# Kernel tuning notes

Measured on AMD Instinct MI355X. Metric: run time of the kernel, lower is better.

Reference implementation:

```python
import jax, jax.numpy as jnp
import numpy as np

B, N, D = 8, 2048, 256
SCALE = 10.0  # self.scale_constant

def setup_inputs() -> dict:
    key = jax.random.key(0)
    ks = jax.random.split(key, 8)
    x = jax.random.normal(ks[0], (B, N, D), dtype=jnp.float32)
    recycler_mask = jax.random.randint(ks[1], (N, N), 0, 2, dtype=jnp.int32)
    s = 1.0 / np.sqrt(D)
    Wq = jax.random.uniform(ks[2], (D, D), jnp.float32, -s, s)
    bq = jax.random.uniform(ks[3], (D,), jnp.float32, -s, s)
    Wk = jax.random.uniform(ks[4], (D, D), jnp.float32, -s, s)
    bk = jax.random.uniform(ks[5], (D,), jnp.float32, -s, s)
    Wl = jax.random.uniform(ks[6], (1, D), jnp.float32, -s, s)
    bl = jax.random.uniform(ks[7], (1,), jnp.float32, -s, s)
    return {"x": x, "recycler_mask": recycler_mask, "Wq": Wq, "bq": bq,
            "Wk": Wk, "bk": bk, "Wl": Wl, "bl": bl}

def reference(x, recycler_mask, Wq, bq, Wk, bk, Wl, bl):
    # query/key linear projections (torch Linear: x @ W.T + b)
    query = jnp.einsum('bnd,ed->bne', x, Wq) + bq  # (B,N,D)
    key_ = jnp.einsum('bnd,ed->bne', x, Wk) + bk   # (B,N,D)
    scores = jnp.einsum('bnd,bmd->bnm', query, key_)  # (B,N,N)
    scores = SCALE * jnp.tanh(scores)
    scores = jnp.where(recycler_mask[None, :, :] == 0, -jnp.inf, scores)
    picked_logit = jnp.einsum('bnd,ed->bne', x, Wl) + bl  # (B,N,1)
    return picked_logit, scores
```

## Files before the change

### kernel.cpp

```cpp
#include <hip/hip_runtime.h>
#include <math.h>

#define B_ 8
#define N_ 2048
#define D_ 256
#define SCALE_ 10.0f
#define NEG_SENTINEL_ (-1.0e30f)

#define BM 128
#define BN 128
#define BK 64
#define KTILES (D_ / BK)
#define TILE_ELEMS (BM * BK)

typedef unsigned short ushort_t;
typedef __attribute__((ext_vector_type(8))) short bf16x8;
typedef __attribute__((ext_vector_type(4))) float f32x4;

__device__ __forceinline__ ushort_t f2bf(float f) {
    union { float f; unsigned int u; } a; a.f = f;
    unsigned int r = a.u + 0x7fffu + ((a.u >> 16) & 1u);
    return (ushort_t)(r >> 16);
}

__device__ __forceinline__ void gl16(const void* g, void* l) {
    __builtin_amdgcn_global_load_lds(
        (const __attribute__((address_space(1))) unsigned int*)g,
        (__attribute__((address_space(3))) unsigned int*)l, 16, 0, 0);
}

__global__ __launch_bounds__(256) void rcy_proj_v4(
    const float* __restrict__ x,
    const float* __restrict__ Wq, const float* __restrict__ bq,
    const float* __restrict__ Wk, const float* __restrict__ bk,
    ushort_t* __restrict__ Qo, ushort_t* __restrict__ Ko)
{
    __shared__ ushort_t As[BM * BK];
    __shared__ ushort_t Bs[BN * BK];

    const float* W  = blockIdx.z ? Wk : Wq;
    const float* bi = blockIdx.z ? bk : bq;
    ushort_t* out   = blockIdx.z ? Ko : Qo;

    const int m0 = blockIdx.x * BM;
    const int n0 = blockIdx.y * BN;
    const int t  = threadIdx.x;
    const int w  = t >> 6, l = t & 63;
    const int wr = w >> 1, wc = w & 1;
    const int srow0 = t >> 3;
    const int schunk = t & 7;

    f32x4 acc[4][4] = {};

    for (int k0 = 0; k0 < D_; k0 += BK) {
        __syncthreads();
        #pragma unroll
        for (int p = 0; p < 4; ++p) {
            const int row = p * 32 + srow0;
            const float4* xa = (const float4*)(x + (size_t)(m0 + row) * D_ + k0 + schunk * 8);
            float4 f0 = xa[0], f1 = xa[1];
            union { bf16x8 v; ushort_t u[8]; } pa;
            pa.u[0]=f2bf(f0.x); pa.u[1]=f2bf(f0.y); pa.u[2]=f2bf(f0.z); pa.u[3]=f2bf(f0.w);
            pa.u[4]=f2bf(f1.x); pa.u[5]=f2bf(f1.y); pa.u[6]=f2bf(f1.z); pa.u[7]=f2bf(f1.w);
            const float4* wa = (const float4*)(W + (size_t)(n0 + row) * D_ + k0 + schunk * 8);
            float4 g0 = wa[0], g1 = wa[1];
            union { bf16x8 v; ushort_t u[8]; } pb;
            pb.u[0]=f2bf(g0.x); pb.u[1]=f2bf(g0.y); pb.u[2]=f2bf(g0.z); pb.u[3]=f2bf(g0.w);
            pb.u[4]=f2bf(g1.x); pb.u[5]=f2bf(g1.y); pb.u[6]=f2bf(g1.z); pb.u[7]=f2bf(g1.w);
            const int off = ((row * 128 + schunk * 16) ^ ((row & 7) << 4));
            *(bf16x8*)((char*)As + off) = pa.v;
            *(bf16x8*)((char*)Bs + off) = pb.v;
        }
        __syncthreads();
        #pragma unroll
        for (int ks = 0; ks < 2; ++ks) {
            bf16x8 af[4], bf[4];
            #pragma unroll
            for (int f = 0; f < 4; ++f) {
                const int m = wr * 64 + f * 16 + (l & 15);
                af[f] = *(const bf16x8*)((const char*)As +
                          ((m * 128 + ks * 64 + (l >> 4) * 16) ^ ((m & 7) << 4)));
                const int n = wc * 64 + f * 16 + (l & 15);
                bf[f] = *(const bf16x8*)((const char*)Bs +
                          ((n * 128 + ks * 64 + (l >> 4) * 16) ^ ((n & 7) << 4)));
            }
            #pragma unroll
            for (int i = 0; i < 4; ++i)
                #pragma unroll
                for (int j = 0; j < 4; ++j)
                    acc[i][j] = __builtin_amdgcn_mfma_f32_16x16x32_bf16(af[i], bf[j], acc[i][j], 0, 0, 0);
        }
    }

    const int b  = m0 >> 11;
    const int rb = (m0 & 2047) >> 7;
    const size_t tbase = (((size_t)b * 16 + rb) * KTILES + (blockIdx.y * 2 + wc)) * (size_t)TILE_ELEMS;
    #pragma unroll
    for (int j = 0; j < 4; ++j) {
        const int col = n0 + wc * 64 + j * 16 + (l & 15);
        const float bv = bi[col];
        const int cl = j * 16 + (l & 15);
        #pragma unroll
        for (int i = 0; i < 4; ++i) {
            #pragma unroll
            for (int r = 0; r < 4; ++r) {
                const int rl = wr * 64 + i * 16 + (l >> 4) * 4 + r;
                out[tbase + (size_t)rl * BK + cl] = f2bf(acc[i][j][r] + bv);
            }
        }
    }
}

__global__ __launch_bounds__(256) void rcy_scores_v4(
    const ushort_t* __restrict__ Qt, const ushort_t* __restrict__ Kt,
    const int* __restrict__ mask, float* __restrict__ out)
{
    __shared__ ushort_t lds[2][2][TILE_ELEMS];

    const int bz = blockIdx.z;
    const int bx = blockIdx.x;
    const int by = blockIdx.y;
    const int t  = threadIdx.x;
    const int w  = t >> 6, l = t & 63;
    const int wr = w >> 1, wc = w & 1;

    const char* gA = (const char*)(Qt + (((size_t)bz * 16 + bx) * KTILES) * TILE_ELEMS);
    const char* gB = (const char*)(Kt + (((size_t)bz * 16 + by) * KTILES) * TILE_ELEMS);

    f32x4 acc[4][4] = {};

    #define STAGE(buf, kb) { \
        const char* sa = gA + (size_t)(kb) * (TILE_ELEMS * 2); \
        const char* sb = gB + (size_t)(kb) * (TILE_ELEMS * 2); \
        char* la = (char*)&lds[buf][0][0]; \
        char* lb = (char*)&lds[buf][1][0]; \
        _Pragma("unroll") \
        for (int q = 0; q < 4; ++q) { \
            gl16(sa + q * 4096 + t * 16, la + q * 4096 + t * 16); \
            gl16(sb + q * 4096 + t * 16, lb + q * 4096 + t * 16); \
        } }

    #define COMPUTE(buf) { \
        const ushort_t* As_ = &lds[buf][0][0]; \
        const ushort_t* Bs_ = &lds[buf][1][0]; \
        _Pragma("unroll") \
        for (int ks = 0; ks < 2; ++ks) { \
            bf16x8 af[4], bf[4]; \
            _Pragma("unroll") \
            for (int f = 0; f < 4; ++f) { \
                const int m = wr * 64 + f * 16 + (l & 15); \
                af[f] = *(const bf16x8*)(As_ + m * BK + ks * 32 + (l >> 4) * 8); \
                const int n = wc * 64 + f * 16 + (l & 15); \
                bf[f] = *(const bf16x8*)(Bs_ + n * BK + ks * 32 + (l >> 4) * 8); \
            } \
            _Pragma("unroll") \
            for (int i = 0; i < 4; ++i) \
                _Pragma("unroll") \
                for (int j = 0; j < 4; ++j) \
                    acc[i][j] = __builtin_amdgcn_mfma_f32_16x16x32_bf16(af[i], bf[j], acc[i][j], 0, 0, 0); \
        } }

    STAGE(0, 0);
    __syncthreads();
    STAGE(1, 1);
    COMPUTE(0);
    __syncthreads();
    STAGE(0, 2);
    COMPUTE(1);
    __syncthreads();
    STAGE(1, 3);
    COMPUTE(0);
    __syncthreads();
    COMPUTE(1);

    const int bm0 = bx * BM, bn0 = by * BN;
    float* outb = out + (size_t)bz * N_ * N_;
    #pragma unroll
    for (int i = 0; i < 4; ++i) {
        #pragma unroll
        for (int r = 0; r < 4; ++r) {
            const int row = bm0 + wr * 64 + i * 16 + (l >> 4) * 4 + r;
            #pragma unroll
            for (int j = 0; j < 4; ++j) {
                const int col = bn0 + wc * 64 + j * 16 + (l & 15);
                const int mk = mask[(size_t)row * N_ + col];
                const float v = acc[i][j][r];
                const float e = __expf(v + v);
                const float s = fmaf(-20.0f, __builtin_amdgcn_rcpf(e + 1.0f), SCALE_);
                outb[(size_t)row * N_ + col] = mk ? s : NEG_SENTINEL_;
            }
        }
    }
    #undef STAGE
    #undef COMPUTE
}

__global__ __launch_bounds__(256) void rcy_logit_v2(
    const float* __restrict__ x, const float* __restrict__ Wl,
    const float* __restrict__ bl, float* __restrict__ out)
{
    const int lane = threadIdx.x & 63;
    const int wv   = threadIdx.x >> 6;
    const int row  = (blockIdx.x << 2) + wv;
    const float* xr = x + (size_t)row * D_;
    float4 v = *(const float4*)&xr[lane << 2];
    float4 wt = *(const float4*)&Wl[lane << 2];
    float s = v.x*wt.x + v.y*wt.y + v.z*wt.z + v.w*wt.w;
    #pragma unroll
    for (int off = 32; off > 0; off >>= 1) s += __shfl_down(s, off);
    if (lane == 0) out[row] = s + bl[0];
}

extern "C" void kernel_launch(void* const* d_in, const int* in_sizes, int n_in,
                              void* d_out, int out_size, void* d_ws, size_t ws_size,
                              hipStream_t stream)
{
    const float* x  = (const float*)d_in[0];
    const int* mask = (const int*)d_in[1];
    const float* Wq = (const float*)d_in[2];
    const float* bq = (const float*)d_in[3];
    const float* Wk = (const float*)d_in[4];
    const float* bk = (const float*)d_in[5];
    const float* Wl = (const float*)d_in[6];
    const float* bl = (const float*)d_in[7];

    float* logit  = (float*)d_out;
    float* scores = (float*)d_out + (size_t)B_ * N_;

    ushort_t* Qw = (ushort_t*)d_ws;
    ushort_t* Kw = Qw + (size_t)B_ * 16 * KTILES * TILE_ELEMS;

    rcy_proj_v4<<<dim3((B_*N_)/BM, D_/BN, 2), 256, 0, stream>>>(x, Wq, bq, Wk, bk, Qw, Kw);
    rcy_scores_v4<<<dim3(N_/BM, N_/BN, B_), 256, 0, stream>>>(Qw, Kw, mask, scores);
    rcy_logit_v2<<<dim3((B_*N_)/4), 256, 0, stream>>>(x, Wl, bl, logit);
}
```

Baseline: 67.68 us.

## Fuse Q/K projections and logit into one kernel, reorder scores grid, nontemporal I/O

```diff
diff --git a/kernel.cpp b/kernel.cpp
--- a/kernel.cpp
+++ b/kernel.cpp
@@ -29,18 +29,17 @@
         (__attribute__((address_space(3))) unsigned int*)l, 16, 0, 0);
 }
 
-__global__ __launch_bounds__(256) void rcy_proj_v4(
+__global__ __launch_bounds__(256) void rcy_proj_v5(
     const float* __restrict__ x,
     const float* __restrict__ Wq, const float* __restrict__ bq,
     const float* __restrict__ Wk, const float* __restrict__ bk,
-    ushort_t* __restrict__ Qo, ushort_t* __restrict__ Ko)
+    const float* __restrict__ Wl, const float* __restrict__ bl,
+    ushort_t* __restrict__ Qo, ushort_t* __restrict__ Ko,
+    float* __restrict__ logit)
 {
     __shared__ ushort_t As[BM * BK];
-    __shared__ ushort_t Bs[BN * BK];
-
-    const float* W  = blockIdx.z ? Wk : Wq;
-    const float* bi = blockIdx.z ? bk : bq;
-    ushort_t* out   = blockIdx.z ? Ko : Qo;
+    __shared__ ushort_t Bqs[BN * BK];
+    __shared__ ushort_t Bks[BN * BK];
 
     const int m0 = blockIdx.x * BM;
     const int n0 = blockIdx.y * BN;
@@ -49,46 +48,67 @@
     const int wr = w >> 1, wc = w & 1;
     const int srow0 = t >> 3;
     const int schunk = t & 7;
-
-    f32x4 acc[4][4] = {};
+    const bool do_logit = (blockIdx.y == 0);
+
+    f32x4 accq[4][4] = {};
+    f32x4 acck[4][4] = {};
+    float lacc[4] = {0.f, 0.f, 0.f, 0.f};
 
     for (int k0 = 0; k0 < D_; k0 += BK) {
         __syncthreads();
+        float4 wl0, wl1;
+        if (do_logit) {
+            const float4* wlp = (const float4*)(Wl + k0 + schunk * 8);
+            wl0 = wlp[0]; wl1 = wlp[1];
+        }
         #pragma unroll
         for (int p = 0; p < 4; ++p) {
             const int row = p * 32 + srow0;
+            const int off = ((row * 128 + schunk * 16) ^ ((row & 7) << 4));
             const float4* xa = (const float4*)(x + (size_t)(m0 + row) * D_ + k0 + schunk * 8);
             float4 f0 = xa[0], f1 = xa[1];
             union { bf16x8 v; ushort_t u[8]; } pa;
             pa.u[0]=f2bf(f0.x); pa.u[1]=f2bf(f0.y); pa.u[2]=f2bf(f0.z); pa.u[3]=f2bf(f0.w);
             pa.u[4]=f2bf(f1.x); pa.u[5]=f2bf(f1.y); pa.u[6]=f2bf(f1.z); pa.u[7]=f2bf(f1.w);
-            const float4* wa = (const float4*)(W + (size_t)(n0 + row) * D_ + k0 + schunk * 8);
-            float4 g0 = wa[0], g1 = wa[1];
+            *(bf16x8*)((char*)As + off) = pa.v;
+            if (do_logit) {
+                lacc[p] += f0.x*wl0.x + f0.y*wl0.y + f0.z*wl0.z + f0.w*wl0.w
+                         + f1.x*wl1.x + f1.y*wl1.y + f1.z*wl1.z + f1.w*wl1.w;
+            }
+            const float4* qa = (const float4*)(Wq + (size_t)(n0 + row) * D_ + k0 + schunk * 8);
+            float4 g0 = qa[0], g1 = qa[1];
             union { bf16x8 v; ushort_t u[8]; } pb;
             pb.u[0]=f2bf(g0.x); pb.u[1]=f2bf(g0.y); pb.u[2]=f2bf(g0.z); pb.u[3]=f2bf(g0.w);
             pb.u[4]=f2bf(g1.x); pb.u[5]=f2bf(g1.y); pb.u[6]=f2bf(g1.z); pb.u[7]=f2bf(g1.w);
-            const int off = ((row * 128 + schunk * 16) ^ ((row & 7) << 4));
-            *(bf16x8*)((char*)As + off) = pa.v;
-            *(bf16x8*)((char*)Bs + off) = pb.v;
+            *(bf16x8*)((char*)Bqs + off) = pb.v;
+            const float4* ka = (const float4*)(Wk + (size_t)(n0 + row) * D_ + k0 + schunk * 8);
+            float4 h0 = ka[0], h1 = ka[1];
+            union { bf16x8 v; ushort_t u[8]; } pc;
+            pc.u[0]=f2bf(h0.x); pc.u[1]=f2bf(h0.y); pc.u[2]=f2bf(h0.z); pc.u[3]=f2bf(h0.w);
+            pc.u[4]=f2bf(h1.x); pc.u[5]=f2bf(h1.y); pc.u[6]=f2bf(h1.z); pc.u[7]=f2bf(h1.w);
+            *(bf16x8*)((char*)Bks + off) = pc.v;
         }
         __syncthreads();
         #pragma unroll
         for (int ks = 0; ks < 2; ++ks) {
-            bf16x8 af[4], bf[4];
+            bf16x8 af[4], bqf[4], bkf[4];
             #pragma unroll
             for (int f = 0; f < 4; ++f) {
                 const int m = wr * 64 + f * 16 + (l & 15);
-                af[f] = *(const bf16x8*)((const char*)As +
-                          ((m * 128 + ks * 64 + (l >> 4) * 16) ^ ((m & 7) << 4)));
+                const int aoff = ((m * 128 + ks * 64 + (l >> 4) * 16) ^ ((m & 7) << 4));
+                af[f] = *(const bf16x8*)((const char*)As + aoff);
                 const int n = wc * 64 + f * 16 + (l & 15);
-                bf[f] = *(const bf16x8*)((const char*)Bs +
-                          ((n * 128 + ks * 64 + (l >> 4) * 16) ^ ((n & 7) << 4)));
+                const int boff = ((n * 128 + ks * 64 + (l >> 4) * 16) ^ ((n & 7) << 4));
+                bqf[f] = *(const bf16x8*)((const char*)Bqs + boff);
+                bkf[f] = *(const bf16x8*)((const char*)Bks + boff);
             }
             #pragma unroll
             for (int i = 0; i < 4; ++i)
                 #pragma unroll
-                for (int j = 0; j < 4; ++j)
-                    acc[i][j] = __builtin_amdgcn_mfma_f32_16x16x32_bf16(af[i], bf[j], acc[i][j], 0, 0, 0);
+                for (int j = 0; j < 4; ++j) {
+                    accq[i][j] = __builtin_amdgcn_mfma_f32_16x16x32_bf16(af[i], bqf[j], accq[i][j], 0, 0, 0);
+                    acck[i][j] = __builtin_amdgcn_mfma_f32_16x16x32_bf16(af[i], bkf[j], acck[i][j], 0, 0, 0);
+                }
         }
     }
 
@@ -98,28 +118,44 @@
     #pragma unroll
     for (int j = 0; j < 4; ++j) {
         const int col = n0 + wc * 64 + j * 16 + (l & 15);
-        const float bv = bi[col];
+        const float bvq = bq[col];
+        const float bvk = bk[col];
         const int cl = j * 16 + (l & 15);
         #pragma unroll
         for (int i = 0; i < 4; ++i) {
             #pragma unroll
             for (int r = 0; r < 4; ++r) {
                 const int rl = wr * 64 + i * 16 + (l >> 4) * 4 + r;
-                out[tbase + (size_t)rl * BK + cl] = f2bf(acc[i][j][r] + bv);
-            }
-        }
-    }
-}
-
-__global__ __launch_bounds__(256) void rcy_scores_v4(
+                Qo[tbase + (size_t)rl * BK + cl] = f2bf(accq[i][j][r] + bvq);
+                Ko[tbase + (size_t)rl * BK + cl] = f2bf(acck[i][j][r] + bvk);
+            }
+        }
+    }
+
+    if (do_logit) {
+        const float bl0 = bl[0];
+        #pragma unroll
+        for (int p = 0; p < 4; ++p) {
+            float s = lacc[p];
+            s += __shfl_down(s, 4);
+            s += __shfl_down(s, 2);
+            s += __shfl_down(s, 1);
+            if (schunk == 0) logit[m0 + p * 32 + srow0] = s + bl0;
+        }
+    }
+}
+
+__global__ __launch_bounds__(256) void rcy_scores_v5(
     const ushort_t* __restrict__ Qt, const ushort_t* __restrict__ Kt,
     const int* __restrict__ mask, float* __restrict__ out)
 {
     __shared__ ushort_t lds[2][2][TILE_ELEMS];
 
-    const int bz = blockIdx.z;
-    const int bx = blockIdx.x;
-    const int by = blockIdx.y;
+    const int g  = blockIdx.x;
+    const int bz = g & 7;
+    const int r_ = g >> 3;
+    const int by = r_ >> 4;
+    const int bx = r_ & 15;
     const int t  = threadIdx.x;
     const int w  = t >> 6, l = t & 63;
     const int wr = w >> 1, wc = w & 1;
@@ -183,32 +219,17 @@
             #pragma unroll
             for (int j = 0; j < 4; ++j) {
                 const int col = bn0 + wc * 64 + j * 16 + (l & 15);
-                const int mk = mask[(size_t)row * N_ + col];
+                const int mk = __builtin_nontemporal_load(&mask[(size_t)row * N_ + col]);
                 const float v = acc[i][j][r];
                 const float e = __expf(v + v);
                 const float s = fmaf(-20.0f, __builtin_amdgcn_rcpf(e + 1.0f), SCALE_);
-                outb[(size_t)row * N_ + col] = mk ? s : NEG_SENTINEL_;
+                __builtin_nontemporal_store(mk ? s : NEG_SENTINEL_,
+                                            &outb[(size_t)row * N_ + col]);
             }
         }
     }
     #undef STAGE
     #undef COMPUTE
-}
-
-__global__ __launch_bounds__(256) void rcy_logit_v2(
-    const float* __restrict__ x, const float* __restrict__ Wl,
-    const float* __restrict__ bl, float* __restrict__ out)
-{
-    const int lane = threadIdx.x & 63;
-    const int wv   = threadIdx.x >> 6;
-    const int row  = (blockIdx.x << 2) + wv;
-    const float* xr = x + (size_t)row * D_;
-    float4 v = *(const float4*)&xr[lane << 2];
-    float4 wt = *(const float4*)&Wl[lane << 2];
-    float s = v.x*wt.x + v.y*wt.y + v.z*wt.z + v.w*wt.w;
-    #pragma unroll
-    for (int off = 32; off > 0; off >>= 1) s += __shfl_down(s, off);
-    if (lane == 0) out[row] = s + bl[0];
 }
 
 extern "C" void kernel_launch(void* const* d_in, const int* in_sizes, int n_in,
@@ -230,7 +251,7 @@
     ushort_t* Qw = (ushort_t*)d_ws;
     ushort_t* Kw = Qw + (size_t)B_ * 16 * KTILES * TILE_ELEMS;
 
-    rcy_proj_v4<<<dim3((B_*N_)/BM, D_/BN, 2), 256, 0, stream>>>(x, Wq, bq, Wk, bk, Qw, Kw);
-    rcy_scores_v4<<<dim3(N_/BM, N_/BN, B_), 256, 0, stream>>>(Qw, Kw, mask, scores);
-    rcy_logit_v2<<<dim3((B_*N_)/4), 256, 0, stream>>>(x, Wl, bl, logit);
-}
+    rcy_proj_v5<<<dim3((B_*N_)/BM, D_/BN), 256, 0, stream>>>(
+        x, Wq, bq, Wk, bk, Wl, bl, Qw, Kw, logit);
+    rcy_scores_v5<<<dim3((N_/BM) * (N_/BN) * B_), 256, 0, stream>>>(Qw, Kw, mask, scores);
+}
```

Result: slower. 118.4 us (+74.9%).
